# Kernel tuning notes

Hardware: AMD Instinct MI355X
Metric: run time of the kernel (lower is better)

## Reference

```python
import jax, jax.numpy as jnp
import numpy as np


def setup_inputs() -> dict:
    key = jax.random.key(0)
    k1, k2 = jax.random.split(key)
    B, H, W, C, S = 128, 32, 32, 64, 64
    x = jax.random.normal(k1, (B, H, W, C), dtype=jnp.float32)
    # accumulators are positive linear-space weights (log is taken in forward)
    accumulators = jax.random.uniform(k2, (H, W, C, S), dtype=jnp.float32, minval=1e-4, maxval=1.0)
    return {"x": x, "accumulators": accumulators}


def reference(x, accumulators):
    # x: [B, H, W, C]; accumulators: [H, W, C, S] (positive, linear space)
    log_w = jnp.log(accumulators)
    # normalize weights over the input-channel axis (axis=2), per scope & sum
    log_w = jax.nn.log_softmax(log_w, axis=2)  # [H, W, C, S]
    # stable per-scope log-domain matmul: log(exp(x) @ exp(log_w))
    mx = jnp.max(x, axis=-1, keepdims=True)        # [B, H, W, 1]
    mw = jnp.max(log_w, axis=2)                    # [H, W, S]
    prod = jnp.einsum("bhwc,hwcs->bhws", jnp.exp(x - mx), jnp.exp(log_w - mw[:, :, None, :]))
    out = jnp.log(prod) + mx + mw                  # [B, H, W, S]
    return out
```

## Files before the change

### kernel.cpp

```cpp
#include <hip/hip_runtime.h>


typedef __attribute__((ext_vector_type(8))) short s8v;
typedef __attribute__((ext_vector_type(4))) float f4v;

__device__ __forceinline__ unsigned short f2bf(float f) {
    unsigned int u = __float_as_uint(f);
    u += 0x7FFFu + ((u >> 16) & 1u);
    return (unsigned short)(u >> 16);
}

__global__ __launch_bounds__(256) void sls_kernel(
    const float* __restrict__ x,
    const float* __restrict__ acc,
    float* __restrict__ out)
{
    const int hw   = blockIdx.x;
    const int t    = threadIdx.x;
    const int lane = t & 63;
    const int wave = t >> 6;

    __shared__ s8v   e_sw[1024];
    __shared__ float psum[16][68];
    __shared__ float mx_s[128];
    __shared__ float lsum_s[64];

    const float4* accv = (const float4*)(acc + (size_t)hw * 4096);
    float4 pa0 = accv[t];
    float4 pa1 = accv[t + 256];
    float4 pa2 = accv[t + 512];
    float4 pa3 = accv[t + 768];

    const int b    = t >> 1;
    const int half = t & 1;
    const float4* xrow = (const float4*)(x + ((size_t)b * 1024 + hw) * 64 + half * 32);
    float4 xv[8];
    #pragma unroll
    for (int j = 0; j < 8; ++j) xv[j] = xrow[j];

    const int ni   = wave;
    const int quad = lane >> 4;
    const int nn   = lane & 15;
    float bf_f[2][8];
    #pragma unroll
    for (int ks = 0; ks < 2; ++ks)
        #pragma unroll
        for (int j = 0; j < 8; ++j) {
            int c = ks * 32 + quad * 8 + j;
            bf_f[ks][j] = acc[(size_t)hw * 4096 + c * 64 + ni * 16 + nn];
        }

    float m = fmaxf(fmaxf(xv[0].x, xv[0].y), fmaxf(xv[0].z, xv[0].w));
    #pragma unroll
    for (int j = 1; j < 8; ++j)
        m = fmaxf(m, fmaxf(fmaxf(xv[j].x, xv[j].y), fmaxf(xv[j].z, xv[j].w)));
    m = fmaxf(m, __shfl_xor(m, 1));
    if (half == 0) mx_s[b] = m;

    #pragma unroll
    for (int q = 0; q < 4; ++q) {
        float4 u0 = xv[2 * q], u1 = xv[2 * q + 1];
        s8v pk;
        pk[0] = (short)f2bf(__expf(u0.x - m));
        pk[1] = (short)f2bf(__expf(u0.y - m));
        pk[2] = (short)f2bf(__expf(u0.z - m));
        pk[3] = (short)f2bf(__expf(u0.w - m));
        pk[4] = (short)f2bf(__expf(u1.x - m));
        pk[5] = (short)f2bf(__expf(u1.y - m));
        pk[6] = (short)f2bf(__expf(u1.z - m));
        pk[7] = (short)f2bf(__expf(u1.w - m));
        e_sw[((b >> 4) * 2 + half) * 64 + q * 16 + (b & 15)] = pk;
    }

    float4 p;
    p.x = (pa0.x + pa1.x) + (pa2.x + pa3.x);
    p.y = (pa0.y + pa1.y) + (pa2.y + pa3.y);
    p.z = (pa0.z + pa1.z) + (pa2.z + pa3.z);
    p.w = (pa0.w + pa1.w) + (pa2.w + pa3.w);
    *((float4*)&psum[t >> 4][(t & 15) * 4]) = p;

    __syncthreads();

    if (t < 64) {
        float ssum = 0.f;
        #pragma unroll
        for (int r = 0; r < 16; ++r) ssum += psum[r][t];
        lsum_s[t] = __logf(ssum);
    }
    __syncthreads();

    s8v bfrag0, bfrag1;
    #pragma unroll
    for (int j = 0; j < 8; ++j) bfrag0[j] = (short)f2bf(bf_f[0][j]);
    #pragma unroll
    for (int j = 0; j < 8; ++j) bfrag1[j] = (short)f2bf(bf_f[1][j]);

    const float lsum_n = lsum_s[ni * 16 + nn];
    float* outp = out + (size_t)hw * 64 + ni * 16 + nn;

    #pragma unroll
    for (int mi = 0; mi < 8; ++mi) {
        s8v a0 = e_sw[(mi * 2 + 0) * 64 + lane];
        s8v a1 = e_sw[(mi * 2 + 1) * 64 + lane];
        f4v d = {0.f, 0.f, 0.f, 0.f};
        d = __builtin_amdgcn_mfma_f32_16x16x32_bf16(a0, bfrag0, d, 0, 0, 0);
        d = __builtin_amdgcn_mfma_f32_16x16x32_bf16(a1, bfrag1, d, 0, 0, 0);
        #pragma unroll
        for (int r = 0; r < 4; ++r) {
            int b_row = mi * 16 + quad * 4 + r;
            float val = __logf(d[r]) + mx_s[b_row] - lsum_n;
            outp[(size_t)b_row * 65536] = val;
        }
    }
}

extern "C" void kernel_launch(void* const* d_in, const int* in_sizes, int n_in,
                              void* d_out, int out_size, void* d_ws, size_t ws_size,
                              hipStream_t stream) {
    const float* x   = (const float*)d_in[0];
    const float* acc = (const float*)d_in[1];
    float* out = (float*)d_out;
    (void)in_sizes; (void)n_in; (void)d_ws; (void)ws_size; (void)out_size;
    sls_kernel<<<dim3(1024), dim3(256), 0, stream>>>(x, acc, out);
}
```

Baseline: 99.58 us.

## Drop redundant accumulator reload, compute column sums in registers, coalesce x loads

The kernel no longer loads the full accumulator tile a second time just to form per-sum column totals. Those totals now come from the per-lane B-fragment values, combined with cross-lane shuffles, which removes one shared-memory reduction and one barrier. The x loads are re-mapped so that 16 threads read one 256-byte row. The row max is computed with a 16-lane shuffle reduction, and rows are stored into a padded row-major LDS array. The A fragments are then read from that layout. The cost is more shuffles per element and a different LDS access pattern.

```diff
diff --git a/kernel.cpp b/kernel.cpp
--- a/kernel.cpp
+++ b/kernel.cpp
@@ -18,98 +18,79 @@
     const int hw   = blockIdx.x;
     const int t    = threadIdx.x;
     const int lane = t & 63;
+    const int quad = lane >> 4;
+    const int nn   = lane & 15;
     const int wave = t >> 6;
 
-    __shared__ s8v   e_sw[1024];
-    __shared__ float psum[16][68];
+    __shared__ unsigned short e_lds[128 * 72];
     __shared__ float mx_s[128];
-    __shared__ float lsum_s[64];
 
-    const float4* accv = (const float4*)(acc + (size_t)hw * 4096);
-    float4 pa0 = accv[t];
-    float4 pa1 = accv[t + 256];
-    float4 pa2 = accv[t + 512];
-    float4 pa3 = accv[t + 768];
-
-    const int b    = t >> 1;
-    const int half = t & 1;
-    const float4* xrow = (const float4*)(x + ((size_t)b * 1024 + hw) * 64 + half * 32);
+    const int r0 = t >> 4;
+    const int c0 = (t & 15) * 4;
+    const float* xbase = x + (size_t)hw * 64 + c0;
     float4 xv[8];
     #pragma unroll
-    for (int j = 0; j < 8; ++j) xv[j] = xrow[j];
+    for (int it = 0; it < 8; ++it)
+        xv[it] = *(const float4*)(xbase + (size_t)(r0 + 16 * it) * 65536);
 
-    const int ni   = wave;
-    const int quad = lane >> 4;
-    const int nn   = lane & 15;
-    float bf_f[2][8];
+    const int ni = wave;
+    const float* accb = acc + (size_t)hw * 4096 + ni * 16 + nn;
+    float bv[2][8];
     #pragma unroll
     for (int ks = 0; ks < 2; ++ks)
         #pragma unroll
-        for (int j = 0; j < 8; ++j) {
-            int c = ks * 32 + quad * 8 + j;
-            bf_f[ks][j] = acc[(size_t)hw * 4096 + c * 64 + ni * 16 + nn];
-        }
-
-    float m = fmaxf(fmaxf(xv[0].x, xv[0].y), fmaxf(xv[0].z, xv[0].w));
-    #pragma unroll
-    for (int j = 1; j < 8; ++j)
-        m = fmaxf(m, fmaxf(fmaxf(xv[j].x, xv[j].y), fmaxf(xv[j].z, xv[j].w)));
-    m = fmaxf(m, __shfl_xor(m, 1));
-    if (half == 0) mx_s[b] = m;
+        for (int j = 0; j < 8; ++j)
+            bv[ks][j] = accb[(ks * 32 + quad * 8 + j) * 64];
 
     #pragma unroll
-    for (int q = 0; q < 4; ++q) {
-        float4 u0 = xv[2 * q], u1 = xv[2 * q + 1];
-        s8v pk;
-        pk[0] = (short)f2bf(__expf(u0.x - m));
-        pk[1] = (short)f2bf(__expf(u0.y - m));
-        pk[2] = (short)f2bf(__expf(u0.z - m));
-        pk[3] = (short)f2bf(__expf(u0.w - m));
-        pk[4] = (short)f2bf(__expf(u1.x - m));
-        pk[5] = (short)f2bf(__expf(u1.y - m));
-        pk[6] = (short)f2bf(__expf(u1.z - m));
-        pk[7] = (short)f2bf(__expf(u1.w - m));
-        e_sw[((b >> 4) * 2 + half) * 64 + q * 16 + (b & 15)] = pk;
+    for (int it = 0; it < 8; ++it) {
+        float4 v = xv[it];
+        float m = fmaxf(fmaxf(v.x, v.y), fmaxf(v.z, v.w));
+        m = fmaxf(m, __shfl_xor(m, 1));
+        m = fmaxf(m, __shfl_xor(m, 2));
+        m = fmaxf(m, __shfl_xor(m, 4));
+        m = fmaxf(m, __shfl_xor(m, 8));
+        const int row = r0 + 16 * it;
+        if (nn == 0) mx_s[row] = m;
+        ushort4 pk;
+        pk.x = f2bf(__expf(v.x - m));
+        pk.y = f2bf(__expf(v.y - m));
+        pk.z = f2bf(__expf(v.z - m));
+        pk.w = f2bf(__expf(v.w - m));
+        *(ushort4*)&e_lds[row * 72 + c0] = pk;
     }
 
-    float4 p;
-    p.x = (pa0.x + pa1.x) + (pa2.x + pa3.x);
-    p.y = (pa0.y + pa1.y) + (pa2.y + pa3.y);
-    p.z = (pa0.z + pa1.z) + (pa2.z + pa3.z);
-    p.w = (pa0.w + pa1.w) + (pa2.w + pa3.w);
-    *((float4*)&psum[t >> 4][(t & 15) * 4]) = p;
+    float csum = 0.f;
+    #pragma unroll
+    for (int ks = 0; ks < 2; ++ks)
+        #pragma unroll
+        for (int j = 0; j < 8; ++j) csum += bv[ks][j];
+    csum += __shfl_xor(csum, 16);
+    csum += __shfl_xor(csum, 32);
+    const float lsum_n = __logf(csum);
+
+    s8v bf0, bf1;
+    #pragma unroll
+    for (int j = 0; j < 8; ++j) {
+        bf0[j] = (short)f2bf(bv[0][j]);
+        bf1[j] = (short)f2bf(bv[1][j]);
+    }
 
     __syncthreads();
 
-    if (t < 64) {
-        float ssum = 0.f;
-        #pragma unroll
-        for (int r = 0; r < 16; ++r) ssum += psum[r][t];
-        lsum_s[t] = __logf(ssum);
-    }
-    __syncthreads();
-
-    s8v bfrag0, bfrag1;
-    #pragma unroll
-    for (int j = 0; j < 8; ++j) bfrag0[j] = (short)f2bf(bf_f[0][j]);
-    #pragma unroll
-    for (int j = 0; j < 8; ++j) bfrag1[j] = (short)f2bf(bf_f[1][j]);
-
-    const float lsum_n = lsum_s[ni * 16 + nn];
     float* outp = out + (size_t)hw * 64 + ni * 16 + nn;
-
     #pragma unroll
     for (int mi = 0; mi < 8; ++mi) {
-        s8v a0 = e_sw[(mi * 2 + 0) * 64 + lane];
-        s8v a1 = e_sw[(mi * 2 + 1) * 64 + lane];
+        const unsigned short* rowp = &e_lds[(mi * 16 + nn) * 72];
+        s8v a0 = *(const s8v*)(rowp + quad * 8);
+        s8v a1 = *(const s8v*)(rowp + 32 + quad * 8);
         f4v d = {0.f, 0.f, 0.f, 0.f};
-        d = __builtin_amdgcn_mfma_f32_16x16x32_bf16(a0, bfrag0, d, 0, 0, 0);
-        d = __builtin_amdgcn_mfma_f32_16x16x32_bf16(a1, bfrag1, d, 0, 0, 0);
+        d = __builtin_amdgcn_mfma_f32_16x16x32_bf16(a0, bf0, d, 0, 0, 0);
+        d = __builtin_amdgcn_mfma_f32_16x16x32_bf16(a1, bf1, d, 0, 0, 0);
         #pragma unroll
         for (int r = 0; r < 4; ++r) {
-            int b_row = mi * 16 + quad * 4 + r;
-            float val = __logf(d[r]) + mx_s[b_row] - lsum_n;
-            outp[(size_t)b_row * 65536] = val;
+            const int b_row = mi * 16 + quad * 4 + r;
+            outp[(size_t)b_row * 65536] = __logf(d[r]) + mx_s[b_row] - lsum_n;
         }
     }
 }
```

After: 96.53 us. -3.1%, faster.
